# Performance work log

Measured on AMD Instinct MI355X. Metric: run time of the kernel, lower is better.

Reference implementation:

```python
import jax, jax.numpy as jnp
import numpy as np

EMBED_DIM = 1024
BATCH = 4
SEQ = 2048


def setup_inputs() -> dict:
    key = jax.random.key(0)
    ks = jax.random.split(key, 9)
    E = EMBED_DIM
    s = 1.0 / np.sqrt(E)
    inp = {
        "x": jax.random.normal(ks[0], (BATCH, SEQ, E), dtype=jnp.float32),
        "Wq": jax.random.uniform(ks[1], (E, E), jnp.float32, -s, s),
        "bq": jax.random.uniform(ks[2], (E,), jnp.float32, -s, s),
        "Wk": jax.random.uniform(ks[3], (E, E), jnp.float32, -s, s),
        "bk": jax.random.uniform(ks[4], (E,), jnp.float32, -s, s),
        "Wv": jax.random.uniform(ks[5], (E, E), jnp.float32, -s, s),
        "bv": jax.random.uniform(ks[6], (E,), jnp.float32, -s, s),
        "Wo": jax.random.uniform(ks[7], (E, E), jnp.float32, -s, s),
        "bo": jax.random.uniform(ks[8], (E,), jnp.float32, -s, s),
    }
    return inp


def reference(x, Wq, bq, Wk, bk, Wv, bv, Wo, bo):
    # x: [B, S, E]. Single-head attention over full embed_dim.
    scale = x.shape[-1] ** -0.5
    q = jnp.einsum("bse,ef->bsf", x, Wq.T) + bq
    k = jnp.einsum("bse,ef->bsf", x, Wk.T) + bk
    v = jnp.einsum("bse,ef->bsf", x, Wv.T) + bv
    scores = jnp.einsum("bqe,bke->bqk", q, k) * scale  # [B, S, S]
    attn = jax.nn.softmax(scores, axis=-1)             # dropout p=0 -> identity
    out = jnp.einsum("bqk,bke->bqe", attn, v)
    return jnp.einsum("bse,ef->bsf", out, Wo.T) + bo
```

## Files before the change

kernel.cpp:

```cpp
#include <hip/hip_runtime.h>
#include <hip/hip_bf16.h>


typedef __bf16 bf16_t;
typedef __bf16 bf16x8 __attribute__((ext_vector_type(8)));
typedef __bf16 bf16x4 __attribute__((ext_vector_type(4)));
typedef float  f32x16 __attribute__((ext_vector_type(16)));
typedef float  f32x4  __attribute__((ext_vector_type(4)));

__device__ __forceinline__ void async_copy16(const void* g, void* l) {
  __builtin_amdgcn_global_load_lds(
      (const __attribute__((address_space(1))) void*)g,
      (__attribute__((address_space(3))) void*)l, 16, 0, 0);
}

__device__ __forceinline__ void wg_barrier() {
  asm volatile("" ::: "memory");
  __builtin_amdgcn_s_barrier();
  asm volatile("" ::: "memory");
}

__device__ __forceinline__ void lgkm0_fence() {
  asm volatile("s_waitcnt lgkmcnt(0)" ::: "memory");
  __builtin_amdgcn_sched_barrier(0);
}

__device__ __forceinline__ unsigned lds_addr(const void* p) {
  return (unsigned)(unsigned long long)(__attribute__((address_space(3))) const void*)p;
}

__device__ __forceinline__ bf16x8 ds_read128(const bf16_t* p) {
  bf16x8 r;
  asm volatile("ds_read_b128 %0, %1" : "=v"(r) : "v"(lds_addr(p)));
  return r;
}

__device__ __forceinline__ f32x4 mfma16(bf16x8 a, bf16x8 b, f32x4 c) {
  return __builtin_amdgcn_mfma_f32_16x16x32_bf16(a, b, c, 0, 0, 0);
}

__device__ __forceinline__ void store_out(float* p, float v)  { *p = v; }
__device__ __forceinline__ void store_out(bf16_t* p, float v) { *p = (bf16_t)v; }

#define BM 128
#define BN 128
#define BKT 64

template <typename OutT, int NBIAS>
__global__ __launch_bounds__(512, 2) void gemm256_bt(
    const bf16_t* __restrict__ A, const bf16_t* __restrict__ B,
    OutT* __restrict__ C,
    const float* __restrict__ b0, const float* __restrict__ b1,
    const float* __restrict__ b2,
    int M, int N, int K, int lda, int ldb, int ldc, float scale,
    long long strideA, long long strideB, long long strideC) {
  const int z = blockIdx.z;
  A += (long long)z * strideA;
  B += (long long)z * strideB;
  C += (long long)z * strideC;

  int bx = blockIdx.x, by = blockIdx.y;
  {
    const int GX  = gridDim.x;
    const int id  = by * GX + bx;
    const int per = GX * 8;
    const int grp = id / per;
    const int rem = id - grp * per;
    by = grp * 8 + (rem & 7);
    bx = rem >> 3;
  }

  __shared__ __align__(16) bf16_t As[2 * 256 * 64];
  __shared__ __align__(16) bf16_t Bs[2 * 256 * 64];

  const int t    = threadIdx.x;
  const int lane = t & 63;
  const int w    = t >> 6;
  const int wm   = w & 1;
  const int wn   = w >> 1;
  const int g    = lane >> 4;
  const int l7   = lane & 7;
  const int r15  = lane & 15;
  const int tileM = by * 256;
  const int tileN = bx * 256;

  const int row0 = t >> 3;
  const int gcc  = (t & 7) ^ (row0 & 7);
  const int dstb = (t & ~63) * 8;

  const int sw0 = ((0 + g) ^ l7) * 8;
  const int sw1 = ((4 + g) ^ l7) * 8;
  const int aRow = (wm * 128 + r15) * 64;
  const int bRow = (wn * 64 + r15) * 64;

  const int NT = K >> 6;

  f32x4 acc[8][4] = {};

  auto stageA = [&](int kt, int h) {
    const int cb = (kt & 1) * 16384;
    const bf16_t* src =
        A + (long long)(tileM + h * 128 + row0) * lda + kt * 64 + gcc * 8;
    bf16_t* dst = &As[cb + h * 8192 + dstb];
    async_copy16(src, dst);
    async_copy16(src + (long long)64 * lda, dst + 4096);
  };
  auto stageB = [&](int kt, int h) {
    const int cb = (kt & 1) * 16384;
    const bf16_t* src =
        B + (long long)(tileN + h * 128 + row0) * ldb + kt * 64 + gcc * 8;
    bf16_t* dst = &Bs[cb + h * 8192 + dstb];
    async_copy16(src, dst);
    async_copy16(src + (long long)64 * ldb, dst + 4096);
  };

  stageA(0, 0); stageA(0, 1); stageB(0, 0); stageB(0, 1);
  stageB(1, 0); stageB(1, 1); stageA(1, 0); stageA(1, 1);
  asm volatile("s_waitcnt vmcnt(8)" ::: "memory");
  wg_barrier();

  bf16x8 a[4][2], P[2][2], Q[2][2];

#pragma unroll
  for (int j = 0; j < 2; ++j) {
    P[j][0] = ds_read128(&Bs[bRow + j * 1024 + sw0]);
    P[j][1] = ds_read128(&Bs[bRow + j * 1024 + sw1]);
  }

  auto tile_step = [&](int kt, bf16x8 (&bc)[2][2], bf16x8 (&bq)[2][2]) {
    const int cb = (kt & 1) * 16384;
    const int k2 = kt + 2;
    const bf16_t* Ab = &As[cb + aRow];
    const bf16_t* Bb = &Bs[cb + bRow];

#pragma unroll
    for (int i = 0; i < 4; ++i) {
      a[i][0] = ds_read128(Ab + i * 1024 + sw0);
      a[i][1] = ds_read128(Ab + i * 1024 + sw1);
    }
    wg_barrier();
    lgkm0_fence();
    __builtin_amdgcn_s_setprio(1);
#pragma unroll
    for (int s = 0; s < 2; ++s)
#pragma unroll
      for (int i = 0; i < 4; ++i)
#pragma unroll
        for (int j = 0; j < 2; ++j)
          acc[i][j] = mfma16(a[i][s], bc[j][s], acc[i][j]);
    __builtin_amdgcn_s_setprio(0);
    wg_barrier();

#pragma unroll
    for (int j = 0; j < 2; ++j) {
      bq[j][0] = ds_read128(Bb + 2048 + j * 1024 + sw0);
      bq[j][1] = ds_read128(Bb + 2048 + j * 1024 + sw1);
    }
    wg_barrier();
    lgkm0_fence();
    __builtin_amdgcn_s_setprio(1);
#pragma unroll
    for (int s = 0; s < 2; ++s)
#pragma unroll
      for (int i = 0; i < 4; ++i)
#pragma unroll
        for (int j = 0; j < 2; ++j)
          acc[i][2 + j] = mfma16(a[i][s], bq[j][s], acc[i][2 + j]);
    __builtin_amdgcn_s_setprio(0);
    wg_barrier();

#pragma unroll
    for (int i = 0; i < 4; ++i) {
      a[i][0] = ds_read128(Ab + 4096 + i * 1024 + sw0);
      a[i][1] = ds_read128(Ab + 4096 + i * 1024 + sw1);
    }
    if (k2 < NT) { stageB(k2, 0); stageB(k2, 1); }
    wg_barrier();
    lgkm0_fence();
    __builtin_amdgcn_s_setprio(1);
#pragma unroll
    for (int s = 0; s < 2; ++s)
#pragma unroll
      for (int i = 0; i < 4; ++i)
#pragma unroll
        for (int j = 0; j < 2; ++j)
          acc[4 + i][2 + j] = mfma16(a[i][s], bq[j][s], acc[4 + i][2 + j]);
    __builtin_amdgcn_s_setprio(0);
    if (k2 < NT) asm volatile("s_waitcnt vmcnt(4)" ::: "memory");
    else         asm volatile("s_waitcnt vmcnt(0)" ::: "memory");
    wg_barrier();

    if (kt + 1 < NT) {
      const bf16_t* Bn = &Bs[((kt + 1) & 1) * 16384 + bRow];
#pragma unroll
      for (int j = 0; j < 2; ++j) {
        bq[j][0] = ds_read128(Bn + j * 1024 + sw0);
        bq[j][1] = ds_read128(Bn + j * 1024 + sw1);
      }
    }
    if (k2 < NT) { stageA(k2, 0); stageA(k2, 1); }
    __builtin_amdgcn_s_setprio(1);
#pragma unroll
    for (int s = 0; s < 2; ++s)
#pragma unroll
      for (int i = 0; i < 4; ++i)
#pragma unroll
        for (int j = 0; j < 2; ++j)
          acc[4 + i][j] = mfma16(a[i][s], bc[j][s], acc[4 + i][j]);
    __builtin_amdgcn_s_setprio(0);
    wg_barrier();
  };

  for (int kt = 0; kt < NT; kt += 2) {
    tile_step(kt,     P, Q);
    tile_step(kt + 1, Q, P);
  }

  float bvv[4];
#pragma unroll
  for (int j = 0; j < 4; ++j) {
    const int col = tileN + wn * 64 + j * 16 + r15;
    float bv = 0.f;
    if (NBIAS == 1) bv = b0[col];
    if (NBIAS == 3) {
      const float* bp = col < 1024 ? b0 : (col < 2048 ? b1 : b2);
      bv = bp[col & 1023];
    }
    bvv[j] = bv;
  }
#pragma unroll
  for (int i = 0; i < 8; ++i) {
#pragma unroll
    for (int r = 0; r < 4; ++r) {
      const long long row = tileM + wm * 128 + i * 16 + g * 4 + r;
      OutT* Crow = C + row * ldc + tileN + wn * 64 + r15;
#pragma unroll
      for (int j = 0; j < 4; ++j)
        store_out(Crow + j * 16, acc[i][j][r] * scale + bvv[j]);
    }
  }
}

template <typename OutT, int NBIAS>
__global__ __launch_bounds__(256) void gemm_bt(
    const bf16_t* __restrict__ A, const bf16_t* __restrict__ B,
    OutT* __restrict__ C,
    const float* __restrict__ b0, const float* __restrict__ b1,
    const float* __restrict__ b2,
    int M, int N, int K, int lda, int ldb, int ldc, float scale,
    long long strideA, long long strideB, long long strideC) {
  const int z = blockIdx.z;
  A += (long long)z * strideA;
  B += (long long)z * strideB;
  C += (long long)z * strideC;

  int bx = blockIdx.x, by = blockIdx.y;
  {
    const int GX  = gridDim.x;
    const int id  = by * GX + bx;
    const int per = GX * 8;
    const int grp = id / per;
    const int rem = id - grp * per;
    by = grp * 8 + (rem & 7);
    bx = rem >> 3;
  }

  __shared__ __align__(16) bf16_t As[BM * BKT];
  __shared__ __align__(16) bf16_t Bs[BN * BKT];

  const int t    = threadIdx.x;
  const int lane = t & 63;
  const int w    = t >> 6;
  const int wm   = w & 1;
  const int wn   = w >> 1;
  const int tileM = by * BM;
  const int tileN = bx * BN;

  f32x16 acc[2][2] = {};

  for (int k0 = 0; k0 < K; k0 += BKT) {
#pragma unroll
    for (int i = 0; i < 4; ++i) {
      const int c   = t + 256 * i;
      const int row = c >> 3;
      const int cc  = c & 7;
      const int gcc = cc ^ (row & 7);
      const int ldsbase = ((t & ~63) + 256 * i) * 8;
      async_copy16(A + (long long)(tileM + row) * lda + k0 + gcc * 8, &As[ldsbase]);
      async_copy16(B + (long long)(tileN + row) * ldb + k0 + gcc * 8, &Bs[ldsbase]);
    }
    __syncthreads();

#pragma unroll
    for (int s = 0; s < 4; ++s) {
      const int kc = s + 4 * (lane >> 5);
      bf16x8 af[2], bfr[2];
#pragma unroll
      for (int ti = 0; ti < 2; ++ti) {
        const int row = wm * 64 + ti * 32 + (lane & 31);
        af[ti] = *(const bf16x8*)&As[row * BKT + ((kc ^ (row & 7)) * 8)];
      }
#pragma unroll
      for (int tj = 0; tj < 2; ++tj) {
        const int row = wn * 64 + tj * 32 + (lane & 31);
        bfr[tj] = *(const bf16x8*)&Bs[row * BKT + ((kc ^ (row & 7)) * 8)];
      }
#pragma unroll
      for (int ti = 0; ti < 2; ++ti)
#pragma unroll
        for (int tj = 0; tj < 2; ++tj)
          acc[ti][tj] = __builtin_amdgcn_mfma_f32_32x32x16_bf16(
              af[ti], bfr[tj], acc[ti][tj], 0, 0, 0);
    }
    __syncthreads();
  }

#pragma unroll
  for (int tj = 0; tj < 2; ++tj) {
    const int col = tileN + wn * 64 + tj * 32 + (lane & 31);
    float bv = 0.f;
    if (NBIAS == 1) bv = b0[col];
    if (NBIAS == 3) {
      const float* bp = col < 1024 ? b0 : (col < 2048 ? b1 : b2);
      bv = bp[col & 1023];
    }
#pragma unroll
    for (int ti = 0; ti < 2; ++ti) {
      const int rowb = tileM + wm * 64 + ti * 32 + 4 * (lane >> 5);
#pragma unroll
      for (int r = 0; r < 16; ++r) {
        const int row = rowb + (r & 3) + 8 * (r >> 2);
        store_out(&C[(long long)row * ldc + col], acc[ti][tj][r] * scale + bv);
      }
    }
  }
}

__global__ __launch_bounds__(256) void cast_all(
    const float4* __restrict__ w0, const float4* __restrict__ w1,
    const float4* __restrict__ w2, const float4* __restrict__ w3,
    const float4* __restrict__ x,
    bf16x4* __restrict__ wdst, bf16x4* __restrict__ xdst) {
  const int N4W = 1 << 18;
  const int id = blockIdx.x * 256 + threadIdx.x;
  const float4* src;
  bf16x4* dst;
  if (id < 4 * N4W) {
    const int z = id >> 18;
    src = (z == 0 ? w0 : z == 1 ? w1 : z == 2 ? w2 : w3) + (id & (N4W - 1));
    dst = wdst + id;
  } else {
    const int i = id - 4 * N4W;
    src = x + i;
    dst = xdst + i;
  }
  const float4 v = *src;
  bf16x4 o;
  o[0] = (bf16_t)v.x; o[1] = (bf16_t)v.y; o[2] = (bf16_t)v.z; o[3] = (bf16_t)v.w;
  *dst = o;
}

__global__ __launch_bounds__(256) void transpose_bf16(
    const bf16_t* __restrict__ in, bf16_t* __restrict__ out, int R, int C,
    int ldin, long long sIn, long long sOut) {
  in  += (long long)blockIdx.z * sIn;
  out += (long long)blockIdx.z * sOut;
  __shared__ bf16_t tile[32][33];
  const int tx = threadIdx.x, ty = threadIdx.y;
  const int x = blockIdx.x * 32 + tx;
  const int y0 = blockIdx.y * 32;
#pragma unroll
  for (int j = 0; j < 32; j += 8)
    tile[ty + j][tx] = in[(long long)(y0 + ty + j) * ldin + x];
  __syncthreads();
  const int x2 = y0 + tx;
  const int y2 = blockIdx.x * 32;
#pragma unroll
  for (int j = 0; j < 32; j += 8)
    out[(long long)(y2 + ty + j) * R + x2] = tile[tx][ty + j];
}

__global__ __launch_bounds__(256) void softmax_rows(
    const bf16_t* __restrict__ S, bf16_t* __restrict__ P, int cols) {
  const long long row = blockIdx.x;
  const bf16x8* inp = (const bf16x8*)(S + row * cols);
  bf16x8* outp      = (bf16x8*)(P + row * cols);
  const int t = threadIdx.x;
  const int w = t >> 6, lane = t & 63;

  const bf16x8 v = inp[t];
  float f[8];
#pragma unroll
  for (int j = 0; j < 8; ++j) f[j] = (float)v[j];

  float m = f[0];
#pragma unroll
  for (int j = 1; j < 8; ++j) m = fmaxf(m, f[j]);
#pragma unroll
  for (int off = 32; off > 0; off >>= 1) m = fmaxf(m, __shfl_xor(m, off));

  __shared__ float red[8];
  if (lane == 0) red[w] = m;
  __syncthreads();
  m = fmaxf(fmaxf(red[0], red[1]), fmaxf(red[2], red[3]));

  float e[8], sum = 0.f;
#pragma unroll
  for (int j = 0; j < 8; ++j) { e[j] = __expf(f[j] - m); sum += e[j]; }
#pragma unroll
  for (int off = 32; off > 0; off >>= 1) sum += __shfl_xor(sum, off);
  if (lane == 0) red[4 + w] = sum;
  __syncthreads();
  sum = red[4] + red[5] + red[6] + red[7];

  const float inv = 1.f / sum;
  bf16x8 o;
#pragma unroll
  for (int j = 0; j < 8; ++j) o[j] = (bf16_t)(e[j] * inv);
  outp[t] = o;
}

extern "C" void kernel_launch(void* const* d_in, const int* in_sizes, int n_in,
                              void* d_out, int out_size, void* d_ws, size_t ws_size,
                              hipStream_t stream) {
  const int E = 1024, S = 2048, B = 4;
  const int BS = B * S;

  const float* x  = (const float*)d_in[0];
  const float* Wq = (const float*)d_in[1];
  const float* bq = (const float*)d_in[2];
  const float* Wk = (const float*)d_in[3];
  const float* bk = (const float*)d_in[4];
  const float* Wv = (const float*)d_in[5];
  const float* bv = (const float*)d_in[6];
  const float* Wo = (const float*)d_in[7];
  const float* bo = (const float*)d_in[8];
  float* out = (float*)d_out;

  char* w = (char*)d_ws;
  const size_t MB = 1ull << 20;
  bf16_t* Wqkvb = (bf16_t*)(w + 0 * MB);
  bf16_t* Wob   = Wqkvb + 3 * E * E;
  bf16_t* xb    = (bf16_t*)(w + 8 * MB);
  bf16_t* QKVb  = (bf16_t*)(w + 24 * MB);
  bf16_t* VTb   = (bf16_t*)(w + 72 * MB);
  bf16_t* Sb    = (bf16_t*)(w + 88 * MB);
  bf16_t* Pb    = (bf16_t*)(w + 8 * MB);
  bf16_t* Ob    = (bf16_t*)(w + 40 * MB);

  {
    const int totalBlocks = ((4 << 18) + (1 << 21)) / 256;
    cast_all<<<totalBlocks, 256, 0, stream>>>(
        (const float4*)Wq, (const float4*)Wk, (const float4*)Wv,
        (const float4*)Wo, (const float4*)x, (bf16x4*)Wqkvb, (bf16x4*)xb);
  }

  gemm256_bt<bf16_t, 3><<<dim3(3 * E / 256, BS / 256, 1), 512, 0, stream>>>(
      xb, Wqkvb, QKVb, bq, bk, bv,
      BS, 3 * E, E, E, E, 3 * E, 1.f, 0, 0, 0);

  transpose_bf16<<<dim3(E / 32, S / 32, B), dim3(32, 8), 0, stream>>>(
      QKVb + 2 * E, VTb, S, E, 3 * E, (long long)S * 3 * E, (long long)E * S);

  gemm256_bt<bf16_t, 0><<<dim3(S / 256, S / 256, B), 512, 0, stream>>>(
      QKVb, QKVb + E, Sb, nullptr, nullptr, nullptr,
      S, S, E, 3 * E, 3 * E, S, 0.03125f,
      (long long)S * 3 * E, (long long)S * 3 * E, (long long)S * S);

  softmax_rows<<<BS, 256, 0, stream>>>(Sb, Pb, S);

  gemm_bt<bf16_t, 0><<<dim3(E / BN, S / BM, B), 256, 0, stream>>>(
      Pb, VTb, Ob, nullptr, nullptr, nullptr,
      S, E, S, S, S, E, 1.f,
      (long long)S * S, (long long)E * S, (long long)S * E);

  gemm_bt<float, 1><<<dim3(E / BN, BS / BM, 1), 256, 0, stream>>>(
      Ob, Wob, out, bo, nullptr, nullptr,
      BS, E, E, E, E, E, 1.f, 0, 0, 0);
}
```

Measured before the change: 296.1 us.

## Restructure GEMM main loop with one-ahead prefetch and fine-grained LDS waits

Changes the GEMM k-loop from a two-tile-ahead prefetch with four barriers per tile to a one-tile-ahead prefetch with a single barrier per tile. LDS waits are split into partial lgkmcnt counts so MFMAs on early fragments can start before all fragments arrive. Global-to-LDS copies for the next tile are issued earlier inside the step. The intent is to cut barrier stalls and raise MFMA/LDS overlap, at the cost of shorter lookahead for global loads and tighter reliance on exact wait counts, where the async copies may also count against lgkmcnt.

```diff
diff --git a/kernel.cpp b/kernel.cpp
--- a/kernel.cpp
+++ b/kernel.cpp
@@ -20,10 +20,11 @@
   asm volatile("" ::: "memory");
 }
 
-__device__ __forceinline__ void lgkm0_fence() {
-  asm volatile("s_waitcnt lgkmcnt(0)" ::: "memory");
-  __builtin_amdgcn_sched_barrier(0);
-}
+#define LGKM(n)                                                  \
+  do {                                                           \
+    asm volatile("s_waitcnt lgkmcnt(" #n ")" ::: "memory");      \
+    __builtin_amdgcn_sched_barrier(0);                           \
+  } while (0)
 
 __device__ __forceinline__ unsigned lds_addr(const void* p) {
   return (unsigned)(unsigned long long)(__attribute__((address_space(3))) const void*)p;
@@ -45,6 +46,22 @@
 #define BM 128
 #define BN 128
 #define BKT 64
+
+#define G_AQ(i, ro, bb, co)                                                   \
+  acc[(ro) + (i)][(co) + 0] = mfma16(a[i][0], bb[0][0], acc[(ro) + (i)][(co) + 0]); \
+  acc[(ro) + (i)][(co) + 1] = mfma16(a[i][0], bb[1][0], acc[(ro) + (i)][(co) + 1]); \
+  acc[(ro) + (i)][(co) + 0] = mfma16(a[i][1], bb[0][1], acc[(ro) + (i)][(co) + 0]); \
+  acc[(ro) + (i)][(co) + 1] = mfma16(a[i][1], bb[1][1], acc[(ro) + (i)][(co) + 1]);
+
+#define G_BQ(j, bb, co)                                              \
+  acc[0][(co) + (j)] = mfma16(a[0][0], bb[j][0], acc[0][(co) + (j)]); \
+  acc[1][(co) + (j)] = mfma16(a[1][0], bb[j][0], acc[1][(co) + (j)]); \
+  acc[2][(co) + (j)] = mfma16(a[2][0], bb[j][0], acc[2][(co) + (j)]); \
+  acc[3][(co) + (j)] = mfma16(a[3][0], bb[j][0], acc[3][(co) + (j)]); \
+  acc[0][(co) + (j)] = mfma16(a[0][1], bb[j][1], acc[0][(co) + (j)]); \
+  acc[1][(co) + (j)] = mfma16(a[1][1], bb[j][1], acc[1][(co) + (j)]); \
+  acc[2][(co) + (j)] = mfma16(a[2][1], bb[j][1], acc[2][(co) + (j)]); \
+  acc[3][(co) + (j)] = mfma16(a[3][1], bb[j][1], acc[3][(co) + (j)]);
 
 template <typename OutT, int NBIAS>
 __global__ __launch_bounds__(512, 2) void gemm256_bt(
@@ -115,12 +132,10 @@
   };
 
   stageA(0, 0); stageA(0, 1); stageB(0, 0); stageB(0, 1);
-  stageB(1, 0); stageB(1, 1); stageA(1, 0); stageA(1, 1);
-  asm volatile("s_waitcnt vmcnt(8)" ::: "memory");
+  asm volatile("s_waitcnt vmcnt(0)" ::: "memory");
   wg_barrier();
 
   bf16x8 a[4][2], P[2][2], Q[2][2];
-
 #pragma unroll
   for (int j = 0; j < 2; ++j) {
     P[j][0] = ds_read128(&Bs[bRow + j * 1024 + sw0]);
@@ -129,7 +144,7 @@
 
   auto tile_step = [&](int kt, bf16x8 (&bc)[2][2], bf16x8 (&bq)[2][2]) {
     const int cb = (kt & 1) * 16384;
-    const int k2 = kt + 2;
+    const int kn = kt + 1;
     const bf16_t* Ab = &As[cb + aRow];
     const bf16_t* Bb = &Bs[cb + bRow];
 
@@ -138,77 +153,63 @@
       a[i][0] = ds_read128(Ab + i * 1024 + sw0);
       a[i][1] = ds_read128(Ab + i * 1024 + sw1);
     }
-    wg_barrier();
-    lgkm0_fence();
+    if (kn < NT) { stageB(kn, 0); stageB(kn, 1); }
     __builtin_amdgcn_s_setprio(1);
-#pragma unroll
-    for (int s = 0; s < 2; ++s)
-#pragma unroll
-      for (int i = 0; i < 4; ++i)
-#pragma unroll
-        for (int j = 0; j < 2; ++j)
-          acc[i][j] = mfma16(a[i][s], bc[j][s], acc[i][j]);
+    LGKM(6);
+    G_AQ(0, 0, bc, 0)
+    LGKM(4);
+    G_AQ(1, 0, bc, 0)
+    LGKM(2);
+    G_AQ(2, 0, bc, 0)
+    LGKM(0);
+    G_AQ(3, 0, bc, 0)
     __builtin_amdgcn_s_setprio(0);
-    wg_barrier();
 
 #pragma unroll
     for (int j = 0; j < 2; ++j) {
       bq[j][0] = ds_read128(Bb + 2048 + j * 1024 + sw0);
       bq[j][1] = ds_read128(Bb + 2048 + j * 1024 + sw1);
     }
-    wg_barrier();
-    lgkm0_fence();
+    if (kn < NT) { stageA(kn, 0); stageA(kn, 1); }
     __builtin_amdgcn_s_setprio(1);
-#pragma unroll
-    for (int s = 0; s < 2; ++s)
-#pragma unroll
-      for (int i = 0; i < 4; ++i)
-#pragma unroll
-        for (int j = 0; j < 2; ++j)
-          acc[i][2 + j] = mfma16(a[i][s], bq[j][s], acc[i][2 + j]);
+    LGKM(2);
+    G_BQ(0, bq, 2)
+    LGKM(0);
+    G_BQ(1, bq, 2)
     __builtin_amdgcn_s_setprio(0);
-    wg_barrier();
 
 #pragma unroll
     for (int i = 0; i < 4; ++i) {
       a[i][0] = ds_read128(Ab + 4096 + i * 1024 + sw0);
       a[i][1] = ds_read128(Ab + 4096 + i * 1024 + sw1);
     }
-    if (k2 < NT) { stageB(k2, 0); stageB(k2, 1); }
+    __builtin_amdgcn_s_setprio(1);
+    LGKM(6);
+    G_AQ(0, 4, bq, 2)
+    LGKM(4);
+    G_AQ(1, 4, bq, 2)
+    LGKM(2);
+    G_AQ(2, 4, bq, 2)
+    LGKM(0);
+    G_AQ(3, 4, bq, 2)
+    __builtin_amdgcn_s_setprio(0);
+    asm volatile("s_waitcnt vmcnt(0)" ::: "memory");
     wg_barrier();
-    lgkm0_fence();
-    __builtin_amdgcn_s_setprio(1);
-#pragma unroll
-    for (int s = 0; s < 2; ++s)
-#pragma unroll
-      for (int i = 0; i < 4; ++i)
-#pragma unroll
-        for (int j = 0; j < 2; ++j)
-          acc[4 + i][2 + j] = mfma16(a[i][s], bq[j][s], acc[4 + i][2 + j]);
-    __builtin_amdgcn_s_setprio(0);
-    if (k2 < NT) asm volatile("s_waitcnt vmcnt(4)" ::: "memory");
-    else         asm volatile("s_waitcnt vmcnt(0)" ::: "memory");
-    wg_barrier();
-
-    if (kt + 1 < NT) {
-      const bf16_t* Bn = &Bs[((kt + 1) & 1) * 16384 + bRow];
+
+    if (kn < NT) {
+      const bf16_t* Bn = &Bs[(kn & 1) * 16384 + bRow];
 #pragma unroll
       for (int j = 0; j < 2; ++j) {
         bq[j][0] = ds_read128(Bn + j * 1024 + sw0);
         bq[j][1] = ds_read128(Bn + j * 1024 + sw1);
       }
     }
-    if (k2 < NT) { stageA(k2, 0); stageA(k2, 1); }
     __builtin_amdgcn_s_setprio(1);
-#pragma unroll
-    for (int s = 0; s < 2; ++s)
-#pragma unroll
-      for (int i = 0; i < 4; ++i)
-#pragma unroll
-        for (int j = 0; j < 2; ++j)
-          acc[4 + i][j] = mfma16(a[i][s], bc[j][s], acc[4 + i][j]);
+    G_AQ(0, 4, bc, 0)
+    G_AQ(1, 4, bc, 0)
+    G_AQ(2, 4, bc, 0)
+    G_AQ(3, 4, bc, 0)
     __builtin_amdgcn_s_setprio(0);
-    wg_barrier();
   };
 
   for (int kt = 0; kt < NT; kt += 2) {
```

Result: faster. 287.1 us (-3.0%).
